# Kernel optimization log

Hardware: AMD Instinct MI355X
Metric: run time of the kernel (lower is better)

The kernel has to match this reference:

```python
import jax, jax.numpy as jnp
import numpy as np

# config constants (assumed; see notes)
OSC_COUPLING = 0.1
AMP_DECAY = 0.1
AMP_SAT = 1.0
HOPF_MU = 1.0
H = 1024
N_OSC = 64  # min(N_OSCILLATORS=64, H//8=128)


def leaky_relu(x, slope=0.2):
    return jnp.where(x >= 0, x, slope * x)


def setup_inputs() -> dict:
    key = jax.random.key(0)
    ks = jax.random.split(key, 16)
    B, S = 4, 2048
    sc_h = 1.0 / np.sqrt(H)
    sc_2n = 1.0 / np.sqrt(2 * N_OSC)
    return {
        "x": jax.random.normal(ks[0], (B, S, H), jnp.float32),
        "t": jax.random.uniform(ks[1], (B, S, 1), jnp.float32),
        # to_oscillator: Linear(H,H) -> LeakyReLU -> Linear(H, 2*N_OSC)
        "W1": jax.random.normal(ks[2], (H, H), jnp.float32) * sc_h,
        "b1": jnp.zeros((H,), jnp.float32),
        "W2": jax.random.normal(ks[3], (H, 2 * N_OSC), jnp.float32) * sc_h,
        "b2": jnp.zeros((2 * N_OSC,), jnp.float32),
        # from_oscillator: Linear(2*N_OSC,H) -> LeakyReLU -> Linear(H,H)
        "W3": jax.random.normal(ks[4], (2 * N_OSC, H), jnp.float32) * sc_2n,
        "b3": jnp.zeros((H,), jnp.float32),
        "W4": jax.random.normal(ks[5], (H, H), jnp.float32) * sc_h,
        "b4": jnp.zeros((H,), jnp.float32),
        # time_mod: Linear(1, N_OSC)
        "Wt": jax.random.normal(ks[6], (1, N_OSC), jnp.float32),
        "bt": jnp.zeros((N_OSC,), jnp.float32),
        "coupling": jax.random.normal(ks[7], (N_OSC, N_OSC), jnp.float32) * OSC_COUPLING,
        "frequencies": jnp.linspace(0.5, 2.0, N_OSC, dtype=jnp.float32),
        "mu": jnp.float32(HOPF_MU),
    }


def reference(x, t, W1, b1, W2, b2, W3, b3, W4, b4, Wt, bt, coupling, frequencies, mu):
    n = frequencies.shape[0]
    # to_oscillator MLP
    h = leaky_relu(x @ W1 + b1)
    osc = h @ W2 + b2                       # [B,S,2n]
    phase, amplitude = osc[..., :n], osc[..., n:]
    t_mod = t @ Wt + bt                      # [B,S,n]

    # NOTE: original loop reads phase[:, i-1] / amplitude[:, i-1] from the
    # ORIGINAL tensors, so steps are independent -> vectorize over time.
    pp = phase[:, :-1]                       # [B,S-1,n] prev phase
    diff = pp[..., :, None] - pp[..., None, :]   # [B,S-1,n,n]
    # sum over last dim of sin(diff) @ coupling == einsum with coupling row-sums
    csum = coupling.sum(axis=1)              # [n]
    coupling_sum = jnp.einsum('bsjm,m->bsj', jnp.sin(diff), csum)
    dphase = frequencies + coupling_sum * OSC_COUPLING + t_mod[:, 1:] * 0.1
    phase_new = pp + dphase * 0.1

    ap = amplitude[:, :-1]
    damp = (-AMP_DECAY + mu) * ap - ap ** 3
    amp_new = jnp.tanh(ap + damp * 0.1) * AMP_SAT

    phase_out = jnp.concatenate([phase[:, :1], phase_new], axis=1)
    amp_out = jnp.concatenate([amplitude[:, :1], amp_new], axis=1)
    combined = jnp.concatenate([phase_out, amp_out], axis=-1)  # [B,S,2n]

    # from_oscillator MLP
    h2 = leaky_relu(combined @ W3 + b3)
    oscillator_output = h2 @ W4 + b4
    return x + oscillator_output * 0.1
```

## Files before the change

### kernel.cpp

```cpp
#include <hip/hip_runtime.h>
#include <hip/hip_bf16.h>

typedef __hip_bfloat16 bf16;
typedef __attribute__((ext_vector_type(4))) float f32x4;
typedef __attribute__((ext_vector_type(8))) short short8;

#define BM 128
#define BN 128
#define BK 64
#define MROWS 8192
#define PARTSZ (MROWS * 128)

__device__ __forceinline__ void gload_lds16(const void* g, void* l) {
  __builtin_amdgcn_global_load_lds((const __attribute__((address_space(1))) void*)g,
                                   (__attribute__((address_space(3))) void*)l, 16, 0, 0);
}

template<int EPI, bool SWZ>
__global__ __launch_bounds__(256)
void gemm_kernel(const bf16* __restrict__ A, const bf16* __restrict__ Bt,
                 const float* __restrict__ bias, const float* __restrict__ X,
                 void* __restrict__ Cout, int M, int N, int K, int kLen)
{
  __shared__ bf16 As[BM * BK];
  __shared__ bf16 Bs[BN * BK];
  const int tid  = threadIdx.x;
  const int lane = tid & 63;
  const int wr   = (tid >> 6) >> 1;
  const int wc   = (tid >> 6) & 1;

  int bmI, bnI;
  if (SWZ) {
    const int nwg = gridDim.x * gridDim.y;
    const int bid = blockIdx.x + gridDim.x * blockIdx.y;
    const int cpx = nwg >> 3;
    const int swz = (bid & 7) * cpx + (bid >> 3);
    bmI = swz % gridDim.x;
    bnI = swz / gridDim.x;
  } else {
    bmI = blockIdx.x;
    bnI = blockIdx.y;
  }
  const long bm = (long)bmI * BM;
  const long bn = (long)bnI * BN;
  const int kOff = blockIdx.z * kLen;

  f32x4 acc[4][4] = {};

  int frow[4], fcol[4], fdst[4];
#pragma unroll
  for (int c = 0; c < 4; ++c) {
    int f    = (c * 256 + tid) * 16;
    int row  = f >> 7;
    int bcol = (f & 127) ^ ((row & 7) << 4);
    frow[c] = row;
    fcol[c] = bcol >> 1;
    fdst[c] = f;
  }

  const int nK = kLen / BK;
  for (int kt = 0; kt < nK; ++kt) {
    const int kb = kOff + kt * BK;
    __syncthreads();
#pragma unroll
    for (int c = 0; c < 4; ++c) {
      gload_lds16(A  + (bm + frow[c]) * (long)K + kb + fcol[c], (char*)As + fdst[c]);
      gload_lds16(Bt + (bn + frow[c]) * (long)K + kb + fcol[c], (char*)Bs + fdst[c]);
    }
    __syncthreads();

#pragma unroll
    for (int ks = 0; ks < 2; ++ks) {
      short8 af[4], bfr[4];
      const int kcolb = (ks * 32 + (lane >> 4) * 8) * 2;
#pragma unroll
      for (int m = 0; m < 4; ++m) {
        int rr = wr * 64 + m * 16 + (lane & 15);
        af[m] = *(const short8*)((const char*)As + rr * 128 + (kcolb ^ ((rr & 7) << 4)));
      }
#pragma unroll
      for (int n = 0; n < 4; ++n) {
        int rr = wc * 64 + n * 16 + (lane & 15);
        bfr[n] = *(const short8*)((const char*)Bs + rr * 128 + (kcolb ^ ((rr & 7) << 4)));
      }
#pragma unroll
      for (int m = 0; m < 4; ++m)
#pragma unroll
        for (int n = 0; n < 4; ++n)
          acc[m][n] = __builtin_amdgcn_mfma_f32_16x16x32_bf16(af[m], bfr[n], acc[m][n], 0, 0, 0);
    }
  }

  char* Cbase = (char*)Cout;
  if (EPI == 1) Cbase += (size_t)blockIdx.z * M * (size_t)N * 4;
#pragma unroll
  for (int n = 0; n < 4; ++n) {
    const long col = bn + wc * 64 + n * 16 + (lane & 15);
    const float bv = (EPI == 1) ? 0.f : bias[col];
#pragma unroll
    for (int m = 0; m < 4; ++m) {
      const long row0 = bm + wr * 64 + m * 16 + ((lane >> 4) << 2);
#pragma unroll
      for (int q = 0; q < 4; ++q) {
        float v = acc[m][n][q] + bv;
        const long idx = (row0 + q) * (long)N + col;
        if (EPI == 0) {
          v = (v >= 0.f) ? v : 0.2f * v;
          ((bf16*)Cbase)[idx] = __float2bfloat16(v);
        } else if (EPI == 1) {
          ((float*)Cbase)[idx] = v;
        } else {
          ((float*)Cbase)[idx] = X[idx] + 0.1f * v;
        }
      }
    }
  }
}

__global__ void convert_bf16_kernel(const float* __restrict__ in, bf16* __restrict__ out, int n4)
{
  int i = blockIdx.x * blockDim.x + threadIdx.x;
  const int stride = gridDim.x * blockDim.x;
  for (; i < n4; i += stride) {
    const float4 v = ((const float4*)in)[i];
    union { bf16 b[4]; uint2 u; } pk;
    pk.b[0] = __float2bfloat16(v.x); pk.b[1] = __float2bfloat16(v.y);
    pk.b[2] = __float2bfloat16(v.z); pk.b[3] = __float2bfloat16(v.w);
    ((uint2*)out)[i] = pk.u;
  }
}

__global__ void transpose_f32_bf16(const float* __restrict__ in, bf16* __restrict__ out,
                                   int R, int C)
{
  __shared__ float tile[32][33];
  const int bx = blockIdx.x * 32;
  const int by = blockIdx.y * 32;
  const int tx = threadIdx.x, ty = threadIdx.y;
#pragma unroll
  for (int i = ty; i < 32; i += 8)
    tile[i][tx] = in[(size_t)(by + i) * C + bx + tx];
  __syncthreads();
#pragma unroll
  for (int i = ty; i < 32; i += 8)
    out[(size_t)(bx + i) * R + by + tx] = __float2bfloat16(tile[tx][i]);
}

__global__ void csum_kernel(const float* __restrict__ coupling, float* __restrict__ csum)
{
  const int m = threadIdx.x;
  float s = 0.f;
#pragma unroll
  for (int n = 0; n < 64; ++n) s += coupling[m * 64 + n];
  csum[m] = s;
}

__global__ void middle_kernel(const float* __restrict__ osc_part, const float* __restrict__ t,
                              const float* __restrict__ Wt, const float* __restrict__ bt,
                              const float* __restrict__ freq, const float* __restrict__ csum,
                              const float* __restrict__ mu_p, const float* __restrict__ b2,
                              bf16* __restrict__ combined, int nrows, int S)
{
  const int r = blockIdx.x * 4 + (threadIdx.x >> 6);
  const int j = threadIdx.x & 63;
  if (r >= nrows) return;
  const int s = r & (S - 1);
  const int src = (s == 0) ? r : r - 1;
  const size_t rs = (size_t)src * 128;

  float p = b2[j], a = b2[64 + j];
#pragma unroll
  for (int kc = 0; kc < 4; ++kc) {
    p += osc_part[(size_t)kc * PARTSZ + rs + j];
    a += osc_part[(size_t)kc * PARTSZ + rs + 64 + j];
  }

  float ph, am;
  if (s == 0) {
    ph = p; am = a;
  } else {
    float sp, cp;
    sincosf(p, &sp, &cp);
    const float cw = csum[j];
    float sumc = cp * cw, sums = sp * cw;
#pragma unroll
    for (int off = 32; off; off >>= 1) {
      sumc += __shfl_xor(sumc, off);
      sums += __shfl_xor(sums, off);
    }
    const float coupling_sum = sp * sumc - cp * sums;
    const float tm = t[r] * Wt[j] + bt[j];
    const float dp = freq[j] + coupling_sum * 0.1f + tm * 0.1f;
    ph = p + dp * 0.1f;
    const float mu = mu_p[0];
    const float u = a + 0.1f * ((mu - 0.1f) * a - a * a * a);
    am = tanhf(u);
  }
  combined[(size_t)r * 128 + j]      = __float2bfloat16(ph);
  combined[(size_t)r * 128 + 64 + j] = __float2bfloat16(am);
}

extern "C" void kernel_launch(void* const* d_in, const int* in_sizes, int n_in,
                              void* d_out, int out_size, void* d_ws, size_t ws_size,
                              hipStream_t stream)
{
  const float* x        = (const float*)d_in[0];
  const float* t        = (const float*)d_in[1];
  const float* W1       = (const float*)d_in[2];
  const float* b1       = (const float*)d_in[3];
  const float* W2       = (const float*)d_in[4];
  const float* b2       = (const float*)d_in[5];
  const float* W3       = (const float*)d_in[6];
  const float* b3       = (const float*)d_in[7];
  const float* W4       = (const float*)d_in[8];
  const float* b4       = (const float*)d_in[9];
  const float* Wt       = (const float*)d_in[10];
  const float* bt       = (const float*)d_in[11];
  const float* coupling = (const float*)d_in[12];
  const float* freq     = (const float*)d_in[13];
  const float* mu       = (const float*)d_in[14];

  const int Mrows = MROWS;
  const int S     = 2048;

  char* ws = (char*)d_ws;
  size_t o = 0;
  auto alloc = [&](size_t bytes) {
    char* p = ws + o;
    o = (o + bytes + 255) & ~(size_t)255;
    return p;
  };
  bf16* xw_h2    = (bf16*)alloc((size_t)Mrows * 1024 * 2);
  bf16* hbuf     = (bf16*)alloc((size_t)Mrows * 1024 * 2);
  bf16* W1t      = (bf16*)alloc((size_t)1024 * 1024 * 2);
  bf16* W4t      = (bf16*)alloc((size_t)1024 * 1024 * 2);
  bf16* W2t      = (bf16*)alloc((size_t)1024 * 128 * 2);
  bf16* W3t      = (bf16*)alloc((size_t)1024 * 128 * 2);
  float* oscp    = (float*)alloc((size_t)4 * PARTSZ * 4);
  bf16* combined = (bf16*)alloc((size_t)Mrows * 128 * 2);
  float* csum    = (float*)alloc(64 * 4);

  convert_bf16_kernel<<<2048, 256, 0, stream>>>(x, xw_h2, Mrows * 1024 / 4);
  transpose_f32_bf16<<<dim3(32, 32), dim3(32, 8), 0, stream>>>(W1, W1t, 1024, 1024);
  transpose_f32_bf16<<<dim3(4, 32),  dim3(32, 8), 0, stream>>>(W2, W2t, 1024, 128);
  transpose_f32_bf16<<<dim3(32, 4),  dim3(32, 8), 0, stream>>>(W3, W3t, 128, 1024);
  transpose_f32_bf16<<<dim3(32, 32), dim3(32, 8), 0, stream>>>(W4, W4t, 1024, 1024);
  csum_kernel<<<1, 64, 0, stream>>>(coupling, csum);

  gemm_kernel<0, true><<<dim3(64, 8), 256, 0, stream>>>(xw_h2, W1t, b1, nullptr, hbuf,
                                                        Mrows, 1024, 1024, 1024);
  gemm_kernel<1, false><<<dim3(64, 1, 4), 256, 0, stream>>>(hbuf, W2t, nullptr, nullptr, oscp,
                                                            Mrows, 128, 1024, 256);
  middle_kernel<<<Mrows / 4, 256, 0, stream>>>(oscp, t, Wt, bt, freq, csum, mu, b2,
                                               combined, Mrows, S);
  gemm_kernel<0, true><<<dim3(64, 8), 256, 0, stream>>>(combined, W3t, b3, nullptr, xw_h2,
                                                        Mrows, 1024, 128, 128);
  gemm_kernel<2, true><<<dim3(64, 8), 256, 0, stream>>>(xw_h2, W4t, b4, x, d_out,
                                                        Mrows, 1024, 1024, 1024);
}
```

Before: 208.9 us.

## Double-buffer GEMM LDS tiles and merge prep kernels into one launch

The GEMM main loop now uses two LDS buffers and issues the global-to-LDS loads for the next K tile before computing the current one. It waits with partial vmcnt counters and raw s_barrier calls in place of the two full __syncthreads per iteration. Separately, the bf16 conversion, the four weight transposes and the coupling row-sum are merged into a single prep kernel, cutting launch count. The doubled LDS footprint (64KB per block) may reduce occupancy, and the hand-placed waitcnt/barrier ordering is fragile.

```diff
diff --git a/kernel.cpp b/kernel.cpp
--- a/kernel.cpp
+++ b/kernel.cpp
@@ -22,8 +22,8 @@
                  const float* __restrict__ bias, const float* __restrict__ X,
                  void* __restrict__ Cout, int M, int N, int K, int kLen)
 {
-  __shared__ bf16 As[BM * BK];
-  __shared__ bf16 Bs[BN * BK];
+  __shared__ bf16 As[2][BM * BK];
+  __shared__ bf16 Bs[2][BN * BK];
   const int tid  = threadIdx.x;
   const int lane = tid & 63;
   const int wr   = (tid >> 6) >> 1;
@@ -58,16 +58,33 @@
     fdst[c] = f;
   }
 
+  const bf16* Abase = A  + bm * (long)K + kOff;
+  const bf16* Bbase = Bt + bn * (long)K + kOff;
+
+#define STAGE(kt, buf)                                                          \
+  do {                                                                          \
+    const long kb_ = (long)(kt) * BK;                                           \
+    _Pragma("unroll")                                                           \
+    for (int c = 0; c < 4; ++c) {                                               \
+      gload_lds16(Abase + (long)frow[c] * K + kb_ + fcol[c],                    \
+                  (char*)As[buf] + fdst[c]);                                    \
+      gload_lds16(Bbase + (long)frow[c] * K + kb_ + fcol[c],                    \
+                  (char*)Bs[buf] + fdst[c]);                                    \
+    }                                                                           \
+  } while (0)
+
   const int nK = kLen / BK;
+  STAGE(0, 0);
   for (int kt = 0; kt < nK; ++kt) {
-    const int kb = kOff + kt * BK;
-    __syncthreads();
-#pragma unroll
-    for (int c = 0; c < 4; ++c) {
-      gload_lds16(A  + (bm + frow[c]) * (long)K + kb + fcol[c], (char*)As + fdst[c]);
-      gload_lds16(Bt + (bn + frow[c]) * (long)K + kb + fcol[c], (char*)Bs + fdst[c]);
-    }
-    __syncthreads();
+    const int cur = kt & 1;
+    if (kt + 1 < nK) {
+      STAGE(kt + 1, cur ^ 1);
+      asm volatile("s_waitcnt vmcnt(8)" ::: "memory");
+    } else {
+      asm volatile("s_waitcnt vmcnt(0)" ::: "memory");
+    }
+    __builtin_amdgcn_s_barrier();
+    __builtin_amdgcn_sched_barrier(0);
 
 #pragma unroll
     for (int ks = 0; ks < 2; ++ks) {
@@ -76,12 +93,12 @@
 #pragma unroll
       for (int m = 0; m < 4; ++m) {
         int rr = wr * 64 + m * 16 + (lane & 15);
-        af[m] = *(const short8*)((const char*)As + rr * 128 + (kcolb ^ ((rr & 7) << 4)));
+        af[m] = *(const short8*)((const char*)As[cur] + rr * 128 + (kcolb ^ ((rr & 7) << 4)));
       }
 #pragma unroll
       for (int n = 0; n < 4; ++n) {
         int rr = wc * 64 + n * 16 + (lane & 15);
-        bfr[n] = *(const short8*)((const char*)Bs + rr * 128 + (kcolb ^ ((rr & 7) << 4)));
+        bfr[n] = *(const short8*)((const char*)Bs[cur] + rr * 128 + (kcolb ^ ((rr & 7) << 4)));
       }
 #pragma unroll
       for (int m = 0; m < 4; ++m)
@@ -89,7 +106,9 @@
         for (int n = 0; n < 4; ++n)
           acc[m][n] = __builtin_amdgcn_mfma_f32_16x16x32_bf16(af[m], bfr[n], acc[m][n], 0, 0, 0);
     }
-  }
+    __builtin_amdgcn_s_barrier();
+  }
+#undef STAGE
 
   char* Cbase = (char*)Cout;
   if (EPI == 1) Cbase += (size_t)blockIdx.z * M * (size_t)N * 4;
@@ -117,42 +136,59 @@
   }
 }
 
-__global__ void convert_bf16_kernel(const float* __restrict__ in, bf16* __restrict__ out, int n4)
-{
-  int i = blockIdx.x * blockDim.x + threadIdx.x;
-  const int stride = gridDim.x * blockDim.x;
-  for (; i < n4; i += stride) {
-    const float4 v = ((const float4*)in)[i];
-    union { bf16 b[4]; uint2 u; } pk;
-    pk.b[0] = __float2bfloat16(v.x); pk.b[1] = __float2bfloat16(v.y);
-    pk.b[2] = __float2bfloat16(v.z); pk.b[3] = __float2bfloat16(v.w);
-    ((uint2*)out)[i] = pk.u;
-  }
-}
-
-__global__ void transpose_f32_bf16(const float* __restrict__ in, bf16* __restrict__ out,
-                                   int R, int C)
+__device__ __forceinline__ void transpose_tile(const float* __restrict__ in,
+                                               bf16* __restrict__ out,
+                                               int R, int C, int bx, int by, int tid)
 {
   __shared__ float tile[32][33];
-  const int bx = blockIdx.x * 32;
-  const int by = blockIdx.y * 32;
-  const int tx = threadIdx.x, ty = threadIdx.y;
+  const int tx = tid & 31, ty = tid >> 5;
 #pragma unroll
   for (int i = ty; i < 32; i += 8)
-    tile[i][tx] = in[(size_t)(by + i) * C + bx + tx];
+    tile[i][tx] = in[(size_t)(by * 32 + i) * C + bx * 32 + tx];
   __syncthreads();
 #pragma unroll
   for (int i = ty; i < 32; i += 8)
-    out[(size_t)(bx + i) * R + by + tx] = __float2bfloat16(tile[tx][i]);
-}
-
-__global__ void csum_kernel(const float* __restrict__ coupling, float* __restrict__ csum)
-{
-  const int m = threadIdx.x;
-  float s = 0.f;
-#pragma unroll
-  for (int n = 0; n < 64; ++n) s += coupling[m * 64 + n];
-  csum[m] = s;
+    out[(size_t)(bx * 32 + i) * R + by * 32 + tx] = __float2bfloat16(tile[tx][i]);
+}
+
+__global__ void prep_kernel(const float* __restrict__ x, bf16* __restrict__ xb,
+                            const float* __restrict__ W1, bf16* __restrict__ W1t,
+                            const float* __restrict__ W2, bf16* __restrict__ W2t,
+                            const float* __restrict__ W3, bf16* __restrict__ W3t,
+                            const float* __restrict__ W4, bf16* __restrict__ W4t,
+                            const float* __restrict__ coupling, float* __restrict__ csum)
+{
+  const int b = blockIdx.x;
+  const int tid = threadIdx.x;
+  if (b < 2048) {
+    const int n4 = MROWS * 1024 / 4;
+    for (int i = b * 256 + tid; i < n4; i += 2048 * 256) {
+      const float4 v = ((const float4*)x)[i];
+      union { bf16 h[4]; uint2 u; } pk;
+      pk.h[0] = __float2bfloat16(v.x); pk.h[1] = __float2bfloat16(v.y);
+      pk.h[2] = __float2bfloat16(v.z); pk.h[3] = __float2bfloat16(v.w);
+      ((uint2*)xb)[i] = pk.u;
+    }
+  } else if (b < 3072) {
+    const int tb = b - 2048;
+    transpose_tile(W1, W1t, 1024, 1024, tb & 31, tb >> 5, tid);
+  } else if (b < 4096) {
+    const int tb = b - 3072;
+    transpose_tile(W4, W4t, 1024, 1024, tb & 31, tb >> 5, tid);
+  } else if (b < 4224) {
+    const int tb = b - 4096;
+    transpose_tile(W2, W2t, 1024, 128, tb & 3, tb >> 2, tid);
+  } else if (b < 4352) {
+    const int tb = b - 4224;
+    transpose_tile(W3, W3t, 128, 1024, tb & 31, tb >> 5, tid);
+  } else {
+    if (tid < 64) {
+      float s = 0.f;
+#pragma unroll
+      for (int n = 0; n < 64; ++n) s += coupling[tid * 64 + n];
+      csum[tid] = s;
+    }
+  }
 }
 
 __global__ void middle_kernel(const float* __restrict__ osc_part, const float* __restrict__ t,
@@ -240,12 +276,8 @@
   bf16* combined = (bf16*)alloc((size_t)Mrows * 128 * 2);
   float* csum    = (float*)alloc(64 * 4);
 
-  convert_bf16_kernel<<<2048, 256, 0, stream>>>(x, xw_h2, Mrows * 1024 / 4);
-  transpose_f32_bf16<<<dim3(32, 32), dim3(32, 8), 0, stream>>>(W1, W1t, 1024, 1024);
-  transpose_f32_bf16<<<dim3(4, 32),  dim3(32, 8), 0, stream>>>(W2, W2t, 1024, 128);
-  transpose_f32_bf16<<<dim3(32, 4),  dim3(32, 8), 0, stream>>>(W3, W3t, 128, 1024);
-  transpose_f32_bf16<<<dim3(32, 32), dim3(32, 8), 0, stream>>>(W4, W4t, 1024, 1024);
-  csum_kernel<<<1, 64, 0, stream>>>(coupling, csum);
+  prep_kernel<<<4353, 256, 0, stream>>>(x, xw_h2, W1, W1t, W2, W2t, W3, W3t, W4, W4t,
+                                        coupling, csum);
 
   gemm_kernel<0, true><<<dim3(64, 8), 256, 0, stream>>>(xw_h2, W1t, b1, nullptr, hbuf,
                                                         Mrows, 1024, 1024, 1024);
```

After: 192.0 us. -8.1%, faster.
